# Optimization experiments

Hardware: AMD Instinct MI355X
Metric: run time of the kernel (lower is better)

The kernel has to match this reference:

```python
import jax, jax.numpy as jnp
import numpy as np

Q, N, D, C = 2048, 32768, 512, 100


def setup_inputs() -> dict:
    key = jax.random.key(0)
    k1, k2, k3 = jax.random.split(key, 3)
    x = jax.random.normal(k1, (Q, D), dtype=jnp.float32)
    embeddings_db = jax.random.normal(k2, (N, D), dtype=jnp.float32)
    labels = jax.random.randint(k3, (N,), 0, C, dtype=jnp.int32)
    return {"x": x, "embeddings_db": embeddings_db, "labels": labels,
            "num_classes": C}


def reference(x, embeddings_db, labels, num_classes):
    # Euclidean cdist via the GEMM form: ||a-b||^2 = ||a||^2 + ||b||^2 - 2 a.b
    x2 = jnp.sum(x * x, axis=1)                      # [Q]
    db2 = jnp.sum(embeddings_db * embeddings_db, 1)  # [N]
    d2 = x2[:, None] + db2[None, :] - 2.0 * (x @ embeddings_db.T)  # [Q, N]
    dist = jnp.sqrt(jnp.maximum(d2, 0.0))            # [Q, N]
    # Per-class (segmented) min over the database axis.
    # Empty segments yield +inf, matching the torch.inf fill in the original.
    min_d = jax.ops.segment_min(dist.T, labels, num_segments=num_classes).T  # [Q, C]
    return -min_d
```

## Files before the change

### kernel.cpp

```cpp
#include <hip/hip_runtime.h>

#define QN 2048
#define NN 32768
#define DD 512
#define CC 100
#define NG32 1124
#define MAXTILES 282
#define NHB 32
#define PADBIG (1 << 29)

typedef int i32x4 __attribute__((ext_vector_type(4)));
typedef float f32x4 __attribute__((ext_vector_type(4)));

#define M_HIST 0
#define M_SEG 128
#define M_TC32 256
#define M_NT 1504
#define M_NCOL 1505
#define M_BH 1536
#define M_BB 5632

#define OFF_X2 65536u
#define OFF_DB2 131072u
#define OFF_XB 524288u
#define OFF_SLAB 3145728u
#define OFF_DBS 13631488u

__device__ __forceinline__ int q8(float v) {
  return (int)rintf(fminf(fmaxf(v * 16.f, -127.f), 127.f));
}

typedef const __attribute__((address_space(1))) void* gptr_t;
typedef __attribute__((address_space(3))) void* lptr_t;
__device__ __forceinline__ void gload_lds16(const void* g, void* l) {
  __builtin_amdgcn_global_load_lds((gptr_t)g, (lptr_t)l, 16, 0, 0);
}

__global__ void k_prep(const float* __restrict__ x, const int* __restrict__ labels,
                       char* __restrict__ xb, int* __restrict__ x2i,
                       int* __restrict__ meta) {
  __shared__ int h[CC];
  int b = blockIdx.x, t = threadIdx.x;
  if (b >= QN / 4) {
    int bb = b - QN / 4;
    if (t < CC) h[t] = 0;
    __syncthreads();
#pragma unroll
    for (int i = 0; i < 4; ++i) atomicAdd(&h[labels[bb * 1024 + i * 256 + t]], 1);
    __syncthreads();
    if (t < CC) {
      atomicAdd(&meta[M_HIST + t], h[t]);
      meta[M_BH + bb * 128 + t] = h[t];
    }
    return;
  }
  int w = t >> 6, lane = t & 63;
  int q = b * 4 + w;
  const float4* row = (const float4*)(x + (size_t)q * DD);
  float4 v0 = row[lane * 2];
  float4 v1 = row[lane * 2 + 1];
  int q0 = q8(v0.x), q1 = q8(v0.y), q2 = q8(v0.z), q3 = q8(v0.w);
  int q4 = q8(v1.x), q5 = q8(v1.y), q6 = q8(v1.z), q7 = q8(v1.w);
  unsigned lo = (q0 & 255) | ((q1 & 255) << 8) | ((q2 & 255) << 16) | ((q3 & 255) << 24);
  unsigned hi = (q4 & 255) | ((q5 & 255) << 8) | ((q6 & 255) << 16) | ((q7 & 255) << 24);
  ((unsigned long long*)(xb + (size_t)q * DD))[lane] =
      (unsigned long long)lo | ((unsigned long long)hi << 32);
  int s = q0 * q0 + q1 * q1 + q2 * q2 + q3 * q3 + q4 * q4 + q5 * q5 + q6 * q6 + q7 * q7;
#pragma unroll
  for (int m = 32; m; m >>= 1) s += __shfl_xor(s, m);
  if (lane == 0) x2i[q] = s;
}

__global__ void k_scan(int* __restrict__ meta) {
  __shared__ int h[CC], s32[CC];
  int t = threadIdx.x;
  if (t < CC) h[t] = meta[M_HIST + t];
  __syncthreads();
  if (t == 0) {
    int col = 0;
    for (int c = 0; c < CC; ++c) {
      s32[c] = col;
      col += ((h[c] + 31) >> 5) << 5;
    }
    meta[M_NT] = (col + 127) >> 7;
    meta[M_NCOL] = col;
  }
  __syncthreads();
  if (t < CC) {
    meta[M_SEG + t] = s32[t];
    int g0 = s32[t] >> 5, ng = (h[t] + 31) >> 5;
    for (int i = 0; i < ng; ++i) meta[M_TC32 + g0 + i] = t;
    int run = s32[t];
    for (int bb = 0; bb < NHB; ++bb) {
      meta[M_BB + bb * 128 + t] = run;
      run += meta[M_BH + bb * 128 + t];
    }
  }
}

__global__ void k_spi(const float* __restrict__ db, const int* __restrict__ labels,
                      const int* __restrict__ meta, char* __restrict__ dbs,
                      int* __restrict__ db2i) {
  int b = blockIdx.x, t = threadIdx.x;
  int w = t >> 6, lane = t & 63;
  if (b < NN / 4) {
    int n = b * 4 + w;
    int c = labels[n];
    int r0 = (n >> 10) << 10;
    int cnt = 0;
#pragma unroll
    for (int i = 0; i < 16; ++i) {
      int j = r0 + i * 64 + lane;
      unsigned long long bal = __ballot(j < n && labels[j] == c);
      cnt += __popcll(bal);
    }
    int pos = meta[M_BB + (n >> 10) * 128 + c] + cnt;
    const float4* row = (const float4*)(db + (size_t)n * DD);
    float4 v0 = row[lane * 2];
    float4 v1 = row[lane * 2 + 1];
    int q0 = q8(v0.x), q1 = q8(v0.y), q2 = q8(v0.z), q3 = q8(v0.w);
    int q4 = q8(v1.x), q5 = q8(v1.y), q6 = q8(v1.z), q7 = q8(v1.w);
    unsigned lo = (q0 & 255) | ((q1 & 255) << 8) | ((q2 & 255) << 16) | ((q3 & 255) << 24);
    unsigned hi = (q4 & 255) | ((q5 & 255) << 8) | ((q6 & 255) << 16) | ((q7 & 255) << 24);
    ((unsigned long long*)(dbs + (size_t)pos * DD))[lane] =
        (unsigned long long)lo | ((unsigned long long)hi << 32);
    int s = q0 * q0 + q1 * q1 + q2 * q2 + q3 * q3 + q4 * q4 + q5 * q5 + q6 * q6 + q7 * q7;
#pragma unroll
    for (int m = 32; m; m >>= 1) s += __shfl_xor(s, m);
    if (lane == 0) db2i[pos] = s;
  } else {
    int p = (b - NN / 4) * 4 + w;
    if (p >= meta[M_NCOL]) return;
    int c = meta[M_TC32 + (p >> 5)];
    if (p - meta[M_SEG + c] < meta[M_HIST + c]) return;
    ((unsigned long long*)(dbs + (size_t)p * DD))[lane] = 0ull;
    if (lane == 0) db2i[p] = PADBIG;
  }
}

__launch_bounds__(256, 4)
__global__ void k_gemm(const char* __restrict__ xb, const char* __restrict__ dbs,
                       const int* __restrict__ db2i, const int* __restrict__ meta,
                       int* __restrict__ slab) {
  int flat = blockIdx.y * 16 + blockIdx.x;
  int swz = (flat & 7) * (16 * MAXTILES / 8) + (flat >> 3);
  int tq = swz & 15, tn = swz >> 4;
  if (tn >= meta[M_NT]) return;

  __shared__ __align__(16) char SA[128 * 128];
  __shared__ __align__(16) char SB[128 * 128];

  int t = threadIdx.x;
  int lane = t & 63;
  int wid = t >> 6;
  int wm = wid >> 1, wn = wid & 1;
  int cl = lane & 15, g = lane >> 4;

  int trow = t >> 3;
  int gsrc = (t & 7) ^ (trow & 7);
  const char* Ag = xb + ((size_t)(tq * 128 + trow)) * DD + gsrc * 16;
  const char* Bg = dbs + ((size_t)(tn * 128 + trow)) * DD + gsrc * 16;
  int ldst = trow * 128 + (t & 7) * 16;

  int x3 = cl & 7;
  int gk0 = ((0 + g) ^ x3) * 16;
  int gk1 = ((4 + g) ^ x3) * 16;
  int rowA[4], rowB[4];
#pragma unroll
  for (int m = 0; m < 4; ++m) rowA[m] = (wm * 64 + m * 16 + cl) * 128;
#pragma unroll
  for (int n = 0; n < 4; ++n) rowB[n] = (wn * 64 + n * 16 + cl) * 128;

  i32x4 acc[4][4];
#pragma unroll
  for (int m = 0; m < 4; ++m)
#pragma unroll
    for (int n = 0; n < 4; ++n) acc[m][n] = (i32x4){0, 0, 0, 0};

#pragma unroll
  for (int kt = 0; kt < 4; ++kt) {
    int k0 = kt * 128;
#pragma unroll
    for (int u = 0; u < 4; ++u) {
      gload_lds16(Ag + (size_t)u * 32 * DD + k0, &SA[u * 4096 + ldst]);
      gload_lds16(Bg + (size_t)u * 32 * DD + k0, &SB[u * 4096 + ldst]);
    }
    __syncthreads();

    {
      i32x4 a0 = *(const i32x4*)(SA + rowA[0] + gk0);
      i32x4 a1 = *(const i32x4*)(SA + rowA[1] + gk0);
      i32x4 a2 = *(const i32x4*)(SA + rowA[2] + gk0);
      i32x4 a3 = *(const i32x4*)(SA + rowA[3] + gk0);
      i32x4 b0 = *(const i32x4*)(SB + rowB[0] + gk0);
      i32x4 b1 = *(const i32x4*)(SB + rowB[1] + gk0);
      i32x4 b2 = *(const i32x4*)(SB + rowB[2] + gk0);
      i32x4 b3 = *(const i32x4*)(SB + rowB[3] + gk0);
#pragma unroll
      for (int m = 0; m < 4; ++m) {
        i32x4 a = (m == 0) ? a0 : (m == 1) ? a1 : (m == 2) ? a2 : a3;
        acc[m][0] = __builtin_amdgcn_mfma_i32_16x16x64_i8(a, b0, acc[m][0], 0, 0, 0);
        acc[m][1] = __builtin_amdgcn_mfma_i32_16x16x64_i8(a, b1, acc[m][1], 0, 0, 0);
        acc[m][2] = __builtin_amdgcn_mfma_i32_16x16x64_i8(a, b2, acc[m][2], 0, 0, 0);
        acc[m][3] = __builtin_amdgcn_mfma_i32_16x16x64_i8(a, b3, acc[m][3], 0, 0, 0);
      }
    }
    {
      i32x4 a0 = *(const i32x4*)(SA + rowA[0] + gk1);
      i32x4 a1 = *(const i32x4*)(SA + rowA[1] + gk1);
      i32x4 a2 = *(const i32x4*)(SA + rowA[2] + gk1);
      i32x4 a3 = *(const i32x4*)(SA + rowA[3] + gk1);
      i32x4 b0 = *(const i32x4*)(SB + rowB[0] + gk1);
      i32x4 b1 = *(const i32x4*)(SB + rowB[1] + gk1);
      i32x4 b2 = *(const i32x4*)(SB + rowB[2] + gk1);
      i32x4 b3 = *(const i32x4*)(SB + rowB[3] + gk1);
#pragma unroll
      for (int m = 0; m < 4; ++m) {
        i32x4 a = (m == 0) ? a0 : (m == 1) ? a1 : (m == 2) ? a2 : a3;
        acc[m][0] = __builtin_amdgcn_mfma_i32_16x16x64_i8(a, b0, acc[m][0], 0, 0, 0);
        acc[m][1] = __builtin_amdgcn_mfma_i32_16x16x64_i8(a, b1, acc[m][1], 0, 0, 0);
        acc[m][2] = __builtin_amdgcn_mfma_i32_16x16x64_i8(a, b2, acc[m][2], 0, 0, 0);
        acc[m][3] = __builtin_amdgcn_mfma_i32_16x16x64_i8(a, b3, acc[m][3], 0, 0, 0);
      }
    }
    __syncthreads();
  }

  int gb = tn * 4 + wn * 2;
  int db2v[4];
#pragma unroll
  for (int n = 0; n < 4; ++n) db2v[n] = db2i[tn * 128 + wn * 64 + n * 16 + cl];

#pragma unroll
  for (int m = 0; m < 4; ++m) {
    i32x4 va4, vb4;
#pragma unroll
    for (int r = 0; r < 4; ++r) {
      int va = min(db2v[0] - 2 * acc[m][0][r], db2v[1] - 2 * acc[m][1][r]);
      int vb = min(db2v[2] - 2 * acc[m][2][r], db2v[3] - 2 * acc[m][3][r]);
#pragma unroll
      for (int s = 1; s < 16; s <<= 1) {
        va = min(va, __shfl_xor(va, s));
        vb = min(vb, __shfl_xor(vb, s));
      }
      va4[r] = va;
      vb4[r] = vb;
    }
    if (cl == 0) {
      int row0 = tq * 128 + wm * 64 + m * 16 + g * 4;
      *(i32x4*)(slab + (size_t)gb * QN + row0) = va4;
      *(i32x4*)(slab + (size_t)(gb + 1) * QN + row0) = vb4;
    }
  }
}

__global__ void k_final(const int* __restrict__ meta, const int* __restrict__ slab,
                        const int* __restrict__ x2i, float* __restrict__ out) {
  int c = blockIdx.y;
  int q = blockIdx.x * 256 + threadIdx.x;
  int g0 = meta[M_SEG + c] >> 5;
  int ng = (meta[M_HIST + c] + 31) >> 5;
  int v = 0x7F000000;
  const int* p = slab + (size_t)g0 * QN + q;
  for (int i = 0; i < ng; ++i) v = min(v, p[(size_t)i * QN]);
  float r;
  if (ng == 0)
    r = -__builtin_inff();
  else
    r = -sqrtf(fmaxf((float)(x2i[q] + v), 0.0f)) * 0.0625f;
  out[(size_t)q * CC + c] = r;
}

extern "C" void kernel_launch(void* const* d_in, const int* in_sizes, int n_in,
                              void* d_out, int out_size, void* d_ws, size_t ws_size,
                              hipStream_t stream) {
  (void)in_sizes; (void)n_in; (void)out_size; (void)ws_size;
  const float* x = (const float*)d_in[0];
  const float* db = (const float*)d_in[1];
  const int* labels = (const int*)d_in[2];

  char* ws = (char*)d_ws;
  int* meta = (int*)ws;
  int* x2i = (int*)(ws + OFF_X2);
  int* db2i = (int*)(ws + OFF_DB2);
  int* slab = (int*)(ws + OFF_SLAB);
  char* xb = (char*)(ws + OFF_XB);
  char* dbs = (char*)(ws + OFF_DBS);

  hipMemsetAsync(ws, 0, 40960, stream);
  k_prep<<<QN / 4 + NHB, 256, 0, stream>>>(x, labels, xb, x2i, meta);
  k_scan<<<1, 128, 0, stream>>>(meta);
  k_spi<<<NN / 4 + (MAXTILES * 128) / 4, 256, 0, stream>>>(db, labels, meta, dbs, db2i);
  k_gemm<<<dim3(16, MAXTILES), 256, 0, stream>>>(xb, dbs, db2i, meta, slab);
  k_final<<<dim3(QN / 256, CC), 256, 0, stream>>>(meta, slab, x2i, (float*)d_out);
}
```

Measured before the change: 107.2 us.

## Double-buffer int8 GEMM LDS tiles with 64-wide K stages

Replaces the single 128-wide K tile with two 64-wide shared-memory buffers, so the global-to-LDS load of the next K slice is issued while MFMAs run on the current one. The swizzle and row offsets change to fit a 64-byte row stride, and the number of barriers per K pass drops to one. Shared memory use stays the same, but there are now eight smaller stages, each with less work to hide its latency. Whether the async LDS loads actually overlap depends on how gload_lds16 waits.

```diff
diff --git a/kernel.cpp b/kernel.cpp
--- a/kernel.cpp
+++ b/kernel.cpp
@@ -10,7 +10,6 @@
 #define PADBIG (1 << 29)
 
 typedef int i32x4 __attribute__((ext_vector_type(4)));
-typedef float f32x4 __attribute__((ext_vector_type(4)));
 
 #define M_HIST 0
 #define M_SEG 128
@@ -147,8 +146,10 @@
   int tq = swz & 15, tn = swz >> 4;
   if (tn >= meta[M_NT]) return;
 
-  __shared__ __align__(16) char SA[128 * 128];
-  __shared__ __align__(16) char SB[128 * 128];
+  __shared__ __align__(16) char SA0[128 * 64];
+  __shared__ __align__(16) char SA1[128 * 64];
+  __shared__ __align__(16) char SB0[128 * 64];
+  __shared__ __align__(16) char SB1[128 * 64];
 
   int t = threadIdx.x;
   int lane = t & 63;
@@ -156,20 +157,18 @@
   int wm = wid >> 1, wn = wid & 1;
   int cl = lane & 15, g = lane >> 4;
 
-  int trow = t >> 3;
-  int gsrc = (t & 7) ^ (trow & 7);
+  int trow = t >> 2;
+  int gsrc = (t & 3) ^ ((t >> 3) & 3);
   const char* Ag = xb + ((size_t)(tq * 128 + trow)) * DD + gsrc * 16;
   const char* Bg = dbs + ((size_t)(tn * 128 + trow)) * DD + gsrc * 16;
-  int ldst = trow * 128 + (t & 7) * 16;
-
-  int x3 = cl & 7;
-  int gk0 = ((0 + g) ^ x3) * 16;
-  int gk1 = ((4 + g) ^ x3) * 16;
-  int rowA[4], rowB[4];
-#pragma unroll
-  for (int m = 0; m < 4; ++m) rowA[m] = (wm * 64 + m * 16 + cl) * 128;
-#pragma unroll
-  for (int n = 0; n < 4; ++n) rowB[n] = (wn * 64 + n * 16 + cl) * 128;
+  int ldst = t * 16;
+
+  int gk = (g ^ ((cl >> 1) & 3)) * 16;
+  int rofA[4], rofB[4];
+#pragma unroll
+  for (int m = 0; m < 4; ++m) rofA[m] = (wm * 64 + m * 16 + cl) * 64 + gk;
+#pragma unroll
+  for (int n = 0; n < 4; ++n) rofB[n] = (wn * 64 + n * 16 + cl) * 64 + gk;
 
   i32x4 acc[4][4];
 #pragma unroll
@@ -177,54 +176,44 @@
 #pragma unroll
     for (int n = 0; n < 4; ++n) acc[m][n] = (i32x4){0, 0, 0, 0};
 
-#pragma unroll
-  for (int kt = 0; kt < 4; ++kt) {
-    int k0 = kt * 128;
-#pragma unroll
-    for (int u = 0; u < 4; ++u) {
-      gload_lds16(Ag + (size_t)u * 32 * DD + k0, &SA[u * 4096 + ldst]);
-      gload_lds16(Bg + (size_t)u * 32 * DD + k0, &SB[u * 4096 + ldst]);
-    }
-    __syncthreads();
-
-    {
-      i32x4 a0 = *(const i32x4*)(SA + rowA[0] + gk0);
-      i32x4 a1 = *(const i32x4*)(SA + rowA[1] + gk0);
-      i32x4 a2 = *(const i32x4*)(SA + rowA[2] + gk0);
-      i32x4 a3 = *(const i32x4*)(SA + rowA[3] + gk0);
-      i32x4 b0 = *(const i32x4*)(SB + rowB[0] + gk0);
-      i32x4 b1 = *(const i32x4*)(SB + rowB[1] + gk0);
-      i32x4 b2 = *(const i32x4*)(SB + rowB[2] + gk0);
-      i32x4 b3 = *(const i32x4*)(SB + rowB[3] + gk0);
-#pragma unroll
-      for (int m = 0; m < 4; ++m) {
-        i32x4 a = (m == 0) ? a0 : (m == 1) ? a1 : (m == 2) ? a2 : a3;
-        acc[m][0] = __builtin_amdgcn_mfma_i32_16x16x64_i8(a, b0, acc[m][0], 0, 0, 0);
-        acc[m][1] = __builtin_amdgcn_mfma_i32_16x16x64_i8(a, b1, acc[m][1], 0, 0, 0);
-        acc[m][2] = __builtin_amdgcn_mfma_i32_16x16x64_i8(a, b2, acc[m][2], 0, 0, 0);
-        acc[m][3] = __builtin_amdgcn_mfma_i32_16x16x64_i8(a, b3, acc[m][3], 0, 0, 0);
-      }
-    }
-    {
-      i32x4 a0 = *(const i32x4*)(SA + rowA[0] + gk1);
-      i32x4 a1 = *(const i32x4*)(SA + rowA[1] + gk1);
-      i32x4 a2 = *(const i32x4*)(SA + rowA[2] + gk1);
-      i32x4 a3 = *(const i32x4*)(SA + rowA[3] + gk1);
-      i32x4 b0 = *(const i32x4*)(SB + rowB[0] + gk1);
-      i32x4 b1 = *(const i32x4*)(SB + rowB[1] + gk1);
-      i32x4 b2 = *(const i32x4*)(SB + rowB[2] + gk1);
-      i32x4 b3 = *(const i32x4*)(SB + rowB[3] + gk1);
-#pragma unroll
-      for (int m = 0; m < 4; ++m) {
-        i32x4 a = (m == 0) ? a0 : (m == 1) ? a1 : (m == 2) ? a2 : a3;
-        acc[m][0] = __builtin_amdgcn_mfma_i32_16x16x64_i8(a, b0, acc[m][0], 0, 0, 0);
-        acc[m][1] = __builtin_amdgcn_mfma_i32_16x16x64_i8(a, b1, acc[m][1], 0, 0, 0);
-        acc[m][2] = __builtin_amdgcn_mfma_i32_16x16x64_i8(a, b2, acc[m][2], 0, 0, 0);
-        acc[m][3] = __builtin_amdgcn_mfma_i32_16x16x64_i8(a, b3, acc[m][3], 0, 0, 0);
-      }
-    }
-    __syncthreads();
-  }
+#define STAGE(SAx, SBx, KT)                               \
+  gload_lds16(Ag + (KT) * 64, SAx + ldst);                \
+  gload_lds16(Ag + 64 * DD + (KT) * 64, SAx + 4096 + ldst); \
+  gload_lds16(Bg + (KT) * 64, SBx + ldst);                \
+  gload_lds16(Bg + 64 * DD + (KT) * 64, SBx + 4096 + ldst);
+
+#define COMP(SAx, SBx)                                                        \
+  {                                                                           \
+    i32x4 a0 = *(const i32x4*)(SAx + rofA[0]);                                \
+    i32x4 a1 = *(const i32x4*)(SAx + rofA[1]);                                \
+    i32x4 a2 = *(const i32x4*)(SAx + rofA[2]);                                \
+    i32x4 a3 = *(const i32x4*)(SAx + rofA[3]);                                \
+    i32x4 b0 = *(const i32x4*)(SBx + rofB[0]);                                \
+    i32x4 b1 = *(const i32x4*)(SBx + rofB[1]);                                \
+    i32x4 b2 = *(const i32x4*)(SBx + rofB[2]);                                \
+    i32x4 b3 = *(const i32x4*)(SBx + rofB[3]);                                \
+    _Pragma("unroll") for (int m = 0; m < 4; ++m) {                           \
+      i32x4 a = (m == 0) ? a0 : (m == 1) ? a1 : (m == 2) ? a2 : a3;           \
+      acc[m][0] = __builtin_amdgcn_mfma_i32_16x16x64_i8(a, b0, acc[m][0], 0, 0, 0); \
+      acc[m][1] = __builtin_amdgcn_mfma_i32_16x16x64_i8(a, b1, acc[m][1], 0, 0, 0); \
+      acc[m][2] = __builtin_amdgcn_mfma_i32_16x16x64_i8(a, b2, acc[m][2], 0, 0, 0); \
+      acc[m][3] = __builtin_amdgcn_mfma_i32_16x16x64_i8(a, b3, acc[m][3], 0, 0, 0); \
+    }                                                                         \
+  }
+
+  STAGE(SA0, SB0, 0)
+  __syncthreads();
+  STAGE(SA1, SB1, 1) COMP(SA0, SB0) __syncthreads();
+  STAGE(SA0, SB0, 2) COMP(SA1, SB1) __syncthreads();
+  STAGE(SA1, SB1, 3) COMP(SA0, SB0) __syncthreads();
+  STAGE(SA0, SB0, 4) COMP(SA1, SB1) __syncthreads();
+  STAGE(SA1, SB1, 5) COMP(SA0, SB0) __syncthreads();
+  STAGE(SA0, SB0, 6) COMP(SA1, SB1) __syncthreads();
+  STAGE(SA1, SB1, 7) COMP(SA0, SB0) __syncthreads();
+  COMP(SA1, SB1)
+
+#undef STAGE
+#undef COMP
 
   int gb = tn * 4 + wn * 2;
   int db2v[4];
```

After: 106.4 us. About the same (-0.7%).
